# Performance work log

Measured on AMD Instinct MI355X. Metric: run time of the kernel, lower is better.

Reference implementation:

```python
import jax, jax.numpy as jnp
import numpy as np

K_NEIGH = 5          # topk(..., k=5) hardcoded in compute_distance
CLIP = 1.0 - 1e-7    # keep arccos/grad finite under fp roundoff of unit-quat dots


def setup_inputs() -> dict:
    key = jax.random.key(0)
    k1, k2 = jax.random.split(key)
    pose = jax.random.normal(k1, (1024, 21, 4), dtype=jnp.float32)
    tp = jax.random.normal(k2, (10000, 21, 4), dtype=jnp.float32)
    # train_poses are unit quaternions per joint (module assumes pre-normalized bank)
    train_poses = tp / jnp.linalg.norm(tp, axis=-1, keepdims=True)
    return {"pose": pose, "train_poses": train_poses}


def reference(pose, train_poses):
    # F.normalize(pose, dim=2): unit quaternion per joint
    rand = pose / jnp.linalg.norm(pose, axis=-1, keepdims=True)
    # per-joint quaternion dot: [N, M, 21] (avoids the repeat() materialization of the original)
    dots = jnp.einsum('njd,mjd->nmj', rand, train_poses)
    dots = jnp.clip(dots, -CLIP, CLIP)
    # geodesic distance: sum_j arccos(dot_j) / 2  -> [N, M]
    dist = jnp.sum(jnp.arccos(dots), axis=2) * 0.5
    # smallest-5 neighbors along M, then mean -> [N]
    neg_top, _ = jax.lax.top_k(-dist, K_NEIGH)
    dist_vals = jnp.mean(-neg_top, axis=1)
    return dist_vals
```

## Files before the change

kernel.cpp:

```cpp
#include <hip/hip_runtime.h>
#include <math.h>

#define N_POSE   1024
#define M_TRAIN  10000
#define NJOINT   21
#define KNEIGH   5
#define CLIPV    (1.0f - 1e-7f)
#define HPI_F    1.57079632679490f
#define BIGF     1e30f
#define TPB      256
#define QN_FLOATS (N_POSE * NJOINT * 4)

__global__ __launch_bounds__(256)
void pose_norm_kernel(const float* __restrict__ pose, float* __restrict__ qn) {
    int i = blockIdx.x * blockDim.x + threadIdx.x;
    if (i >= N_POSE * NJOINT) return;
    float4 v = ((const float4*)pose)[i];
    float inv = rsqrtf(v.x * v.x + v.y * v.y + v.z * v.z + v.w * v.w);
    v.x *= inv; v.y *= inv; v.z *= inv; v.w *= inv;
    ((float4*)qn)[i] = v;
}

__global__ __launch_bounds__(TPB)
void pose_dist_kernel(const float* __restrict__ qn,
                      const float* __restrict__ train,
                      float* __restrict__ topk,
                      int chunks, int mchunk) {
    const int nb = blockIdx.x / chunks;
    const int cb = blockIdx.x % chunks;
    const int n  = nb * TPB + threadIdx.x;

    float4 q[NJOINT];
    const float4* __restrict__ qp = (const float4*)qn + (size_t)n * NJOINT;
#pragma unroll
    for (int j = 0; j < NJOINT; ++j) q[j] = qp[j];
#pragma unroll
    for (int j = 0; j < NJOINT; ++j)
        asm volatile("" : "+v"(q[j].x), "+v"(q[j].y), "+v"(q[j].z), "+v"(q[j].w));

    float t0 = BIGF, t1 = BIGF, t2 = BIGF, t3 = BIGF, t4 = BIGF;
    const float4* __restrict__ tq = (const float4*)train + (size_t)cb * mchunk * NJOINT;

#pragma unroll 1
    for (int mi = 0; mi < mchunk; ++mi) {
        const float4* __restrict__ tm = tq + (size_t)mi * NJOINT;
        float a0 = 0.f, a1 = 0.f;
#pragma unroll
        for (int j = 0; j < NJOINT; ++j) {
            float4 p = q[j];
            float4 u = tm[j];
            float d = u.x * p.x + u.y * p.y + u.z * p.z + u.w * p.w;
            float a = fminf(fabsf(d), CLIPV);
            float pl = fmaf(a, -0.0187293f, 0.0742610f);
            pl = fmaf(a, pl, -0.2121144f);
            pl = fmaf(a, pl, 1.5707288f);
            float r  = __builtin_amdgcn_sqrtf(1.0f - a) * pl;
            float cs = __builtin_copysignf(HPI_F - r, d);
            if (j & 1) a1 += cs; else a0 += cs;
        }
        float v = (NJOINT * HPI_F - (a0 + a1)) * 0.5f;
        t4 = fminf(t4, fmaxf(t3, v));
        t3 = fminf(t3, fmaxf(t2, v));
        t2 = fminf(t2, fmaxf(t1, v));
        t1 = fminf(t1, fmaxf(t0, v));
        t0 = fminf(t0, v);
    }

    float* w = topk + ((size_t)cb * N_POSE + n) * KNEIGH;
    w[0] = t0; w[1] = t1; w[2] = t2; w[3] = t3; w[4] = t4;
}

__global__ __launch_bounds__(64)
void pose_reduce_kernel(const float* __restrict__ topk, float* __restrict__ out,
                        int chunks) {
    const int n = blockIdx.x;
    const int lane = threadIdx.x;
    const int total = chunks * KNEIGH;

    float t0 = BIGF, t1 = BIGF, t2 = BIGF, t3 = BIGF, t4 = BIGF;
    for (int i = lane; i < total; i += 64) {
        int cb = i / KNEIGH, k = i % KNEIGH;
        float v = topk[((size_t)cb * N_POSE + n) * KNEIGH + k];
        t4 = fminf(t4, fmaxf(t3, v));
        t3 = fminf(t3, fmaxf(t2, v));
        t2 = fminf(t2, fmaxf(t1, v));
        t1 = fminf(t1, fmaxf(t0, v));
        t0 = fminf(t0, v);
    }

    float sum = 0.f;
#pragma unroll
    for (int r = 0; r < KNEIGH; ++r) {
        float v = t0; int who = lane;
        for (int off = 32; off; off >>= 1) {
            float ov = __shfl_xor(v, off);
            int   ow = __shfl_xor(who, off);
            if (ov < v || (ov == v && ow < who)) { v = ov; who = ow; }
        }
        sum += v;
        if (lane == who) { t0 = t1; t1 = t2; t2 = t3; t3 = t4; t4 = BIGF; }
    }
    if (lane == 0) out[n] = sum * (1.0f / KNEIGH);
}

extern "C" void kernel_launch(void* const* d_in, const int* in_sizes, int n_in,
                              void* d_out, int out_size, void* d_ws, size_t ws_size,
                              hipStream_t stream) {
    const float* pose  = (const float*)d_in[0];
    const float* train = (const float*)d_in[1];
    float* out  = (float*)d_out;
    float* qn   = (float*)d_ws;
    float* topk = (float*)d_ws + QN_FLOATS;

    size_t base = (size_t)QN_FLOATS * sizeof(float);
    int chunks = 500;
    if (base + (size_t)N_POSE * chunks * KNEIGH * sizeof(float) > ws_size) chunks = 250;
    if (base + (size_t)N_POSE * chunks * KNEIGH * sizeof(float) > ws_size) chunks = 125;
    if (base + (size_t)N_POSE * chunks * KNEIGH * sizeof(float) > ws_size) chunks = 50;
    if (base + (size_t)N_POSE * chunks * KNEIGH * sizeof(float) > ws_size) chunks = 10;
    const int mchunk = M_TRAIN / chunks;

    pose_norm_kernel<<<dim3((N_POSE * NJOINT + 255) / 256), dim3(256), 0, stream>>>(pose, qn);

    dim3 grid1((N_POSE / TPB) * chunks);
    pose_dist_kernel<<<grid1, dim3(TPB), 0, stream>>>(qn, train, topk, chunks, mchunk);

    pose_reduce_kernel<<<dim3(N_POSE), dim3(64), 0, stream>>>(topk, out, chunks);
}
```

Measured before the change: 111.6 us.

## Split joints across half-waves and combine partial distances with a lane shuffle

Each query pose is now handled by two lanes, 32 apart in the wavefront. One lane covers joints 0-10 and the other covers joints 11-20 plus one duplicated joint that is masked out. The partial arccos sums are combined with a shfl_xor of 32, and only the lower half writes its top-5. The grid doubles, and each thread holds 11 query quaternions instead of 21. This is meant to cut register pressure and raise occupancy and latency hiding. The cost is one wasted joint evaluation and one cross-lane shuffle per training sample.

```diff
diff --git a/kernel.cpp b/kernel.cpp
--- a/kernel.cpp
+++ b/kernel.cpp
@@ -26,29 +26,38 @@
                       const float* __restrict__ train,
                       float* __restrict__ topk,
                       int chunks, int mchunk) {
-    const int nb = blockIdx.x / chunks;
-    const int cb = blockIdx.x % chunks;
-    const int n  = nb * TPB + threadIdx.x;
+    const int nb   = blockIdx.x / chunks;
+    const int cb   = blockIdx.x % chunks;
+    const int tid  = threadIdx.x;
+    const int lane = tid & 63;
+    const int h    = lane >> 5;
+    const int n    = nb * 128 + (tid >> 6) * 32 + (lane & 31);
 
-    float4 q[NJOINT];
-    const float4* __restrict__ qp = (const float4*)qn + (size_t)n * NJOINT;
+    const int voff  = h * 176;
+    const int off10 = voff + (h ? 144 : 160);
+    const float mask10 = h ? 0.f : 1.f;
+
+    float4 q[11];
+    const char* qb = (const char*)qn + (size_t)n * 336;
 #pragma unroll
-    for (int j = 0; j < NJOINT; ++j) q[j] = qp[j];
+    for (int jj = 0; jj < 10; ++jj) q[jj] = *(const float4*)(qb + voff + jj * 16);
+    q[10] = *(const float4*)(qb + off10);
 #pragma unroll
-    for (int j = 0; j < NJOINT; ++j)
-        asm volatile("" : "+v"(q[j].x), "+v"(q[j].y), "+v"(q[j].z), "+v"(q[j].w));
+    for (int jj = 0; jj < 11; ++jj)
+        asm volatile("" : "+v"(q[jj].x), "+v"(q[jj].y), "+v"(q[jj].z), "+v"(q[jj].w));
 
     float t0 = BIGF, t1 = BIGF, t2 = BIGF, t3 = BIGF, t4 = BIGF;
-    const float4* __restrict__ tq = (const float4*)train + (size_t)cb * mchunk * NJOINT;
+    const char* tb = (const char*)train + (size_t)cb * mchunk * 336;
 
 #pragma unroll 1
     for (int mi = 0; mi < mchunk; ++mi) {
-        const float4* __restrict__ tm = tq + (size_t)mi * NJOINT;
+        const char* tm = tb + (size_t)mi * 336;
         float a0 = 0.f, a1 = 0.f;
 #pragma unroll
-        for (int j = 0; j < NJOINT; ++j) {
-            float4 p = q[j];
-            float4 u = tm[j];
+        for (int jj = 0; jj < 11; ++jj) {
+            float4 u = (jj < 10) ? *(const float4*)(tm + voff + jj * 16)
+                                 : *(const float4*)(tm + off10);
+            float4 p = q[jj];
             float d = u.x * p.x + u.y * p.y + u.z * p.z + u.w * p.w;
             float a = fminf(fabsf(d), CLIPV);
             float pl = fmaf(a, -0.0187293f, 0.0742610f);
@@ -56,9 +65,12 @@
             pl = fmaf(a, pl, 1.5707288f);
             float r  = __builtin_amdgcn_sqrtf(1.0f - a) * pl;
             float cs = __builtin_copysignf(HPI_F - r, d);
-            if (j & 1) a1 += cs; else a0 += cs;
+            if (jj == 10) cs *= mask10;
+            if (jj & 1) a1 += cs; else a0 += cs;
         }
-        float v = (NJOINT * HPI_F - (a0 + a1)) * 0.5f;
+        float S = a0 + a1;
+        S += __shfl_xor(S, 32);
+        float v = (NJOINT * HPI_F - S) * 0.5f;
         t4 = fminf(t4, fmaxf(t3, v));
         t3 = fminf(t3, fmaxf(t2, v));
         t2 = fminf(t2, fmaxf(t1, v));
@@ -66,8 +78,10 @@
         t0 = fminf(t0, v);
     }
 
-    float* w = topk + ((size_t)cb * N_POSE + n) * KNEIGH;
-    w[0] = t0; w[1] = t1; w[2] = t2; w[3] = t3; w[4] = t4;
+    if (lane < 32) {
+        float* w = topk + ((size_t)cb * N_POSE + n) * KNEIGH;
+        w[0] = t0; w[1] = t1; w[2] = t2; w[3] = t3; w[4] = t4;
+    }
 }
 
 __global__ __launch_bounds__(64)
@@ -122,7 +136,7 @@
 
     pose_norm_kernel<<<dim3((N_POSE * NJOINT + 255) / 256), dim3(256), 0, stream>>>(pose, qn);
 
-    dim3 grid1((N_POSE / TPB) * chunks);
+    dim3 grid1((N_POSE / 128) * chunks);
     pose_dist_kernel<<<grid1, dim3(TPB), 0, stream>>>(qn, train, topk, chunks, mchunk);
 
     pose_reduce_kernel<<<dim3(N_POSE), dim3(64), 0, stream>>>(topk, out, chunks);
```

New measurement: 151.9 us. 1.36x slower.

## Stream transposed pose rows from memory instead of holding them in registers

Applied to the files above, without the earlier changes.

Pose quaternions are normalized into a transposed layout, 64 rows by joint, so each wave loads its lane's joint quaternion with coalesced loads inside the inner loop instead of keeping 84 registers of query data per thread. Each 256-thread block now covers 64 pose rows, and its four waves split the block's train chunk four ways. Each wave writes its own partial top-5, and the reduce kernel merges four times as many partials. The aim is to cut register pressure and raise occupancy, at the cost of extra L1/LDS-path loads of the query per train item.

```diff
diff --git a/kernel.cpp b/kernel.cpp
--- a/kernel.cpp
+++ b/kernel.cpp
@@ -9,46 +9,51 @@
 #define HPI_F    1.57079632679490f
 #define BIGF     1e30f
 #define TPB      256
-#define QN_FLOATS (N_POSE * NJOINT * 4)
+#define NBROWS   64
+#define MSUB     4
+#define QT_FLOATS (N_POSE * NJOINT * 4)
 
 __global__ __launch_bounds__(256)
-void pose_norm_kernel(const float* __restrict__ pose, float* __restrict__ qn) {
+void pose_norm_t_kernel(const float* __restrict__ pose, float* __restrict__ qT) {
     int i = blockIdx.x * blockDim.x + threadIdx.x;
     if (i >= N_POSE * NJOINT) return;
+    int n = i / NJOINT, j = i % NJOINT;
     float4 v = ((const float4*)pose)[i];
     float inv = rsqrtf(v.x * v.x + v.y * v.y + v.z * v.z + v.w * v.w);
     v.x *= inv; v.y *= inv; v.z *= inv; v.w *= inv;
-    ((float4*)qn)[i] = v;
+    ((float4*)qT)[(((n >> 6) * NJOINT + j) << 6) + (n & 63)] = v;
 }
 
 __global__ __launch_bounds__(TPB)
-void pose_dist_kernel(const float* __restrict__ qn,
+void pose_dist_kernel(const float* __restrict__ qT,
                       const float* __restrict__ train,
                       float* __restrict__ topk,
                       int chunks, int mchunk) {
-    const int nb = blockIdx.x / chunks;
-    const int cb = blockIdx.x % chunks;
-    const int n  = nb * TPB + threadIdx.x;
+    const int nb   = blockIdx.x / chunks;
+    const int cb   = blockIdx.x % chunks;
+    const int wave = threadIdx.x >> 6;
+    const int lane = threadIdx.x & 63;
+    const int n    = nb * NBROWS + lane;
 
-    float4 q[NJOINT];
-    const float4* __restrict__ qp = (const float4*)qn + (size_t)n * NJOINT;
-#pragma unroll
-    for (int j = 0; j < NJOINT; ++j) q[j] = qp[j];
-#pragma unroll
-    for (int j = 0; j < NJOINT; ++j)
-        asm volatile("" : "+v"(q[j].x), "+v"(q[j].y), "+v"(q[j].z), "+v"(q[j].w));
+    const int mq   = mchunk / MSUB;
+    const int mbeg = cb * mchunk + wave * mq;
+
+    uintptr_t qbi = (uintptr_t)(qT + (size_t)nb * (NJOINT * NBROWS * 4));
+    const int vlane = lane * 16;
+    const char* tb = (const char*)train + (size_t)mbeg * 336;
 
     float t0 = BIGF, t1 = BIGF, t2 = BIGF, t3 = BIGF, t4 = BIGF;
-    const float4* __restrict__ tq = (const float4*)train + (size_t)cb * mchunk * NJOINT;
 
 #pragma unroll 1
-    for (int mi = 0; mi < mchunk; ++mi) {
-        const float4* __restrict__ tm = tq + (size_t)mi * NJOINT;
+    for (int mi = 0; mi < mq; ++mi) {
+        asm volatile("" : "+s"(qbi));
+        const char* qc = (const char*)qbi;
+        const float4* __restrict__ tm = (const float4*)(tb + (size_t)mi * 336);
         float a0 = 0.f, a1 = 0.f;
 #pragma unroll
         for (int j = 0; j < NJOINT; ++j) {
-            float4 p = q[j];
             float4 u = tm[j];
+            float4 p = *(const float4*)(qc + j * (NBROWS * 16) + vlane);
             float d = u.x * p.x + u.y * p.y + u.z * p.z + u.w * p.w;
             float a = fminf(fabsf(d), CLIPV);
             float pl = fmaf(a, -0.0187293f, 0.0742610f);
@@ -66,16 +71,16 @@
         t0 = fminf(t0, v);
     }
 
-    float* w = topk + ((size_t)cb * N_POSE + n) * KNEIGH;
+    float* w = topk + ((size_t)(cb * MSUB + wave) * N_POSE + n) * KNEIGH;
     w[0] = t0; w[1] = t1; w[2] = t2; w[3] = t3; w[4] = t4;
 }
 
 __global__ __launch_bounds__(64)
 void pose_reduce_kernel(const float* __restrict__ topk, float* __restrict__ out,
-                        int chunks) {
+                        int chunksEff) {
     const int n = blockIdx.x;
     const int lane = threadIdx.x;
-    const int total = chunks * KNEIGH;
+    const int total = chunksEff * KNEIGH;
 
     float t0 = BIGF, t1 = BIGF, t2 = BIGF, t3 = BIGF, t4 = BIGF;
     for (int i = lane; i < total; i += 64) {
@@ -109,21 +114,20 @@
     const float* pose  = (const float*)d_in[0];
     const float* train = (const float*)d_in[1];
     float* out  = (float*)d_out;
-    float* qn   = (float*)d_ws;
-    float* topk = (float*)d_ws + QN_FLOATS;
+    float* qT   = (float*)d_ws;
+    float* topk = (float*)d_ws + QT_FLOATS;
 
-    size_t base = (size_t)QN_FLOATS * sizeof(float);
-    int chunks = 500;
-    if (base + (size_t)N_POSE * chunks * KNEIGH * sizeof(float) > ws_size) chunks = 250;
-    if (base + (size_t)N_POSE * chunks * KNEIGH * sizeof(float) > ws_size) chunks = 125;
-    if (base + (size_t)N_POSE * chunks * KNEIGH * sizeof(float) > ws_size) chunks = 50;
-    if (base + (size_t)N_POSE * chunks * KNEIGH * sizeof(float) > ws_size) chunks = 10;
+    size_t base = (size_t)QT_FLOATS * sizeof(float);
+    int chunks = 125;
+    if (base + (size_t)chunks * MSUB * N_POSE * KNEIGH * sizeof(float) > ws_size) chunks = 50;
+    if (base + (size_t)chunks * MSUB * N_POSE * KNEIGH * sizeof(float) > ws_size) chunks = 25;
+    if (base + (size_t)chunks * MSUB * N_POSE * KNEIGH * sizeof(float) > ws_size) chunks = 10;
     const int mchunk = M_TRAIN / chunks;
 
-    pose_norm_kernel<<<dim3((N_POSE * NJOINT + 255) / 256), dim3(256), 0, stream>>>(pose, qn);
+    pose_norm_t_kernel<<<dim3((N_POSE * NJOINT + 255) / 256), dim3(256), 0, stream>>>(pose, qT);
 
-    dim3 grid1((N_POSE / TPB) * chunks);
-    pose_dist_kernel<<<grid1, dim3(TPB), 0, stream>>>(qn, train, topk, chunks, mchunk);
+    dim3 grid1((N_POSE / NBROWS) * chunks);
+    pose_dist_kernel<<<grid1, dim3(TPB), 0, stream>>>(qT, train, topk, chunks, mchunk);
 
-    pose_reduce_kernel<<<dim3(N_POSE), dim3(64), 0, stream>>>(topk, out, chunks);
+    pose_reduce_kernel<<<dim3(N_POSE), dim3(64), 0, stream>>>(topk, out, chunks * MSUB);
 }
```

New measurement: 232.9 us. +108.6%, slower.
